# Kernel optimization log

Hardware: AMD Instinct MI355X
Metric: run time of the kernel (lower is better)

The kernel has to match this reference:

```python
import jax, jax.numpy as jnp
import numpy as np

B, C, N = 16, 64, 2048
K, KS, OC = 20, 20, 64
BN_EPS = 1e-5


def setup_inputs() -> dict:
    key = jax.random.key(0)
    k1, k2, k3, k4 = jax.random.split(key, 4)
    feature = jax.random.normal(k1, (B, C, N), dtype=jnp.float32)
    neigh_indexs = jax.random.randint(k2, (B * N, K), 0, B * N, dtype=jnp.int64)
    permatrix = jax.random.normal(k3, (B * N, K, KS), dtype=jnp.float32)
    conv_w = jax.random.normal(k4, (OC, 2 * C), dtype=jnp.float32) * 0.05  # 1x1 conv weight
    conv_b = jnp.zeros((OC,), dtype=jnp.float32)
    gamma = jnp.ones((OC,), dtype=jnp.float32)
    beta = jnp.zeros((OC,), dtype=jnp.float32)
    return {"feature": feature, "neigh_indexs": neigh_indexs, "permatrix": permatrix,
            "conv_w": conv_w, "conv_b": conv_b, "gamma": gamma, "beta": beta}


def _forward(feature, neigh_indexs, permatrix, conv_w, conv_b, gamma, beta):
    bsize, num_feat, num_pts = feature.shape
    # [B, C, N] -> [B*N, C]
    flat = jnp.transpose(feature, (0, 2, 1)).reshape(bsize * num_pts, num_feat)
    # neighbor gather: [B*N, K, C] -> [B*N, C, K]
    feats = jnp.transpose(flat[neigh_indexs], (0, 2, 1))
    f_repeat = jnp.broadcast_to(feats[:, :, 0:1], feats.shape)
    f_relative = feats - f_repeat
    feats = jnp.concatenate([f_repeat, f_relative], axis=1)  # [B*N, 2C, K]
    # per-point small matmul with permutation matrix: [B*N, 2C, KS]
    feats = jnp.einsum('nck,nks->ncs', feats, permatrix)
    # 1x1 conv over channel dim: [B*N, OC, KS]
    out = jnp.einsum('ncs,oc->nos', feats, conv_w) + conv_b[None, :, None]
    # max over neighbors, reshape to [B, OC, N]
    out = jnp.max(out, axis=-1).reshape(bsize, num_pts, -1)
    out = jnp.transpose(out, (0, 2, 1))  # [B, OC, N]
    # BatchNorm1d (training-mode forward: biased var over batch & points)
    mean = jnp.mean(out, axis=(0, 2), keepdims=True)
    var = jnp.var(out, axis=(0, 2), keepdims=True)
    out = (out - mean) * jax.lax.rsqrt(var + BN_EPS)
    return out * gamma[None, :, None] + beta[None, :, None]


def reference(feature, neigh_indexs, permatrix, conv_w, conv_b, gamma, beta):
    return _forward(feature, neigh_indexs, permatrix, conv_w, conv_b, gamma, beta)
```

## Files before the change

### kernel.cpp

```cpp
#include <hip/hip_runtime.h>
#include <hip/hip_fp16.h>

#define B_   16
#define C_   64
#define N_   2048
#define M_   (B_ * N_)
#define K_   20
#define KS_  20
#define OC_  64
#define NWAVE2 8192
#define NBLK2  2048

__global__ __launch_bounds__(256) void k_project(
    const float* __restrict__ feat,
    const float* __restrict__ conv_w,
    __half* __restrict__ ph,
    float*  __restrict__ qf)
{
    const int lane = threadIdx.x & 63;
    const int wg   = blockIdx.x * 4 + (threadIdx.x >> 6);
    float w2[64], wd[64];
    const float4* cw4 = (const float4*)conv_w;
    #pragma unroll
    for (int j = 0; j < 16; ++j) {
        float4 a = cw4[lane * 32 + j];
        float4 b = cw4[lane * 32 + 16 + j];
        w2[4*j+0] = b.x; w2[4*j+1] = b.y; w2[4*j+2] = b.z; w2[4*j+3] = b.w;
        wd[4*j+0] = a.x - b.x; wd[4*j+1] = a.y - b.y;
        wd[4*j+2] = a.z - b.z; wd[4*j+3] = a.w - b.w;
    }
    const int m0 = wg * 16;
    int b0 = m0 >> 11, p0 = m0 & 2047;
    float fv = feat[((size_t)(b0 * 64 + lane)) * 2048 + p0];
    for (int mi = 0; mi < 16; ++mi) {
        const int m = m0 + mi;
        float fnext = 0.f;
        if (mi < 15) {
            const int mn = m + 1;
            fnext = feat[((size_t)((mn >> 11) * 64 + lane)) * 2048 + (mn & 2047)];
        }
        float p0a = 0.f, p1a = 0.f, q0a = 0.f, q1a = 0.f;
        #pragma unroll
        for (int c = 0; c < 32; ++c) {
            float f0 = __int_as_float(
                __builtin_amdgcn_readlane(__float_as_int(fv), c));
            float f1 = __int_as_float(
                __builtin_amdgcn_readlane(__float_as_int(fv), c + 32));
            p0a = fmaf(w2[c], f0, p0a);
            p1a = fmaf(w2[c + 32], f1, p1a);
            q0a = fmaf(wd[c], f0, q0a);
            q1a = fmaf(wd[c + 32], f1, q1a);
        }
        ph[(size_t)m * 64 + lane] = __float2half(p0a + p1a);
        qf[(size_t)m * 64 + lane] = q0a + q1a;
        fv = fnext;
    }
}

typedef float f16v __attribute__((ext_vector_type(16)));

__device__ __forceinline__ float h2f(int u) {
    __half_raw r; r.x = (unsigned short)u;
    return __half2float(__half(r));
}

template<int V, int I>
__device__ __forceinline__ float selv(const f16v& a, const f16v& b,
                                      const f16v& c, const f16v& d,
                                      const f16v& e) {
    if constexpr (V == 0) return a[I];
    else if constexpr (V == 1) return b[I];
    else if constexpr (V == 2) return c[I];
    else if constexpr (V == 3) return d[I];
    else return e[I];
}

template<int KK, bool INIT>
__device__ __forceinline__ void rowfma(float t, float bias, float* acc,
    const f16v& a, const f16v& b, const f16v& c,
    const f16v& d, const f16v& e)
{
    #define RS_(S) { constexpr int e_ = KK * 20 + (S); \
        const float w_ = selv<e_ / 16, e_ % 16>(a, b, c, d, e); \
        acc[S] = fmaf(t, w_, INIT ? bias : acc[S]); }
    RS_(0)  RS_(1)  RS_(2)  RS_(3)  RS_(4)
    RS_(5)  RS_(6)  RS_(7)  RS_(8)  RS_(9)
    RS_(10) RS_(11) RS_(12) RS_(13) RS_(14)
    RS_(15) RS_(16) RS_(17) RS_(18) RS_(19)
    #undef RS_
}

#define CHUNK(tkk, CC, INIT0) { \
    f16v sA, sB, sC, sD, sE; \
    asm volatile("s_load_dwordx16 %0, %1, %2" : "=s"(sA) : "s"(psrc), "n"((CC)*320 +   0)); \
    asm volatile("s_load_dwordx16 %0, %1, %2" : "=s"(sB) : "s"(psrc), "n"((CC)*320 +  64)); \
    asm volatile("s_load_dwordx16 %0, %1, %2" : "=s"(sC) : "s"(psrc), "n"((CC)*320 + 128)); \
    asm volatile("s_load_dwordx16 %0, %1, %2" : "=s"(sD) : "s"(psrc), "n"((CC)*320 + 192)); \
    asm volatile("s_load_dwordx16 %0, %1, %2" : "=s"(sE) : "s"(psrc), "n"((CC)*320 + 256)); \
    asm volatile("s_waitcnt lgkmcnt(0)" \
        : "+s"(sA), "+s"(sB), "+s"(sC), "+s"(sD), "+s"(sE)); \
    rowfma<0, INIT0>(tkk[(CC)*4+0], bias, acc, sA, sB, sC, sD, sE); \
    rowfma<1, false>(tkk[(CC)*4+1], bias, acc, sA, sB, sC, sD, sE); \
    rowfma<2, false>(tkk[(CC)*4+2], bias, acc, sA, sB, sC, sD, sE); \
    rowfma<3, false>(tkk[(CC)*4+3], bias, acc, sA, sB, sC, sD, sE); }

__device__ __forceinline__ void issue_gathers(
    const __half* __restrict__ pht, const float* __restrict__ qft,
    int ivreg, int voff2, int voff4, int (&g)[21])
{
    {
        const int ik0 = __builtin_amdgcn_readlane(ivreg, 0);
        const float* spq = qft + (size_t)(unsigned)ik0 * 64u;
        asm volatile("global_load_dword %0, %1, %2"
                     : "=v"(g[20]) : "v"(voff4), "s"(spq));
    }
    #pragma unroll
    for (int k = 0; k < 20; ++k) {
        const int iku = __builtin_amdgcn_readlane(ivreg, k);
        const __half* sp = pht + (size_t)(unsigned)iku * 64u;
        asm volatile("global_load_ushort %0, %1, %2"
                     : "=v"(g[k]) : "v"(voff2), "s"(sp));
    }
}

#define WAITG(g, CNTTXT) do { \
    asm volatile("s_waitcnt vmcnt(" CNTTXT ")" : \
        "+v"(g[0]),"+v"(g[1]),"+v"(g[2]),"+v"(g[3]),"+v"(g[4]), \
        "+v"(g[5]),"+v"(g[6]),"+v"(g[7]),"+v"(g[8]),"+v"(g[9]), \
        "+v"(g[10]),"+v"(g[11]),"+v"(g[12]),"+v"(g[13]),"+v"(g[14]), \
        "+v"(g[15]),"+v"(g[16]),"+v"(g[17]),"+v"(g[18]),"+v"(g[19]), \
        "+v"(g[20])); \
    __builtin_amdgcn_sched_barrier(0); \
} while (0)

#define COMPUTE(gar, NU) { \
    const float* psrc = perm + (size_t)(NU) * 400; \
    const float qv = __int_as_float(gar[20]); \
    float tk[20]; \
    tk[0]  = h2f(gar[0])  + qv; tk[1]  = h2f(gar[1])  + qv; \
    tk[2]  = h2f(gar[2])  + qv; tk[3]  = h2f(gar[3])  + qv; \
    tk[4]  = h2f(gar[4])  + qv; tk[5]  = h2f(gar[5])  + qv; \
    tk[6]  = h2f(gar[6])  + qv; tk[7]  = h2f(gar[7])  + qv; \
    tk[8]  = h2f(gar[8])  + qv; tk[9]  = h2f(gar[9])  + qv; \
    tk[10] = h2f(gar[10]) + qv; tk[11] = h2f(gar[11]) + qv; \
    tk[12] = h2f(gar[12]) + qv; tk[13] = h2f(gar[13]) + qv; \
    tk[14] = h2f(gar[14]) + qv; tk[15] = h2f(gar[15]) + qv; \
    tk[16] = h2f(gar[16]) + qv; tk[17] = h2f(gar[17]) + qv; \
    tk[18] = h2f(gar[18]) + qv; tk[19] = h2f(gar[19]) + qv; \
    float acc[20]; \
    CHUNK(tk, 0, true) \
    CHUNK(tk, 1, false) \
    CHUNK(tk, 2, false) \
    CHUNK(tk, 3, false) \
    CHUNK(tk, 4, false) \
    float mv = acc[0]; \
    mv = fmaxf(mv, acc[1]);  mv = fmaxf(mv, acc[2]);  mv = fmaxf(mv, acc[3]); \
    mv = fmaxf(mv, acc[4]);  mv = fmaxf(mv, acc[5]);  mv = fmaxf(mv, acc[6]); \
    mv = fmaxf(mv, acc[7]);  mv = fmaxf(mv, acc[8]);  mv = fmaxf(mv, acc[9]); \
    mv = fmaxf(mv, acc[10]); mv = fmaxf(mv, acc[11]); mv = fmaxf(mv, acc[12]); \
    mv = fmaxf(mv, acc[13]); mv = fmaxf(mv, acc[14]); mv = fmaxf(mv, acc[15]); \
    mv = fmaxf(mv, acc[16]); mv = fmaxf(mv, acc[17]); mv = fmaxf(mv, acc[18]); \
    mv = fmaxf(mv, acc[19]); \
    const float* pdst = pre + (size_t)(NU) * 64; \
    asm volatile("global_store_dword %0, %1, %2" \
                 :: "v"(voff4), "v"(mv), "s"(pdst)); \
    sum += mv; \
    sumsq = fmaf(mv, mv, sumsq); }

__global__ __launch_bounds__(256) void k_points(
    const __half* __restrict__ ph,
    const float*  __restrict__ qf,
    const int*    __restrict__ nidx,
    const float*  __restrict__ perm,
    const float*  __restrict__ conv_b,
    float* __restrict__ pre,
    float* __restrict__ partials)
{
    const int tid  = threadIdx.x;
    const int lane = tid & 63;
    const int w    = tid >> 6;
    const int wg   = (int)blockIdx.x * 4 + w;
    const int wgu  = __builtin_amdgcn_readfirstlane(wg);
    const int voff4 = lane * 4;
    const int voff2 = lane * 2;

    float bias = conv_b[lane];
    float sum = 0.f, sumsq = 0.f;

    int iv0 = 0, iv1 = 0, iv2 = 0, iv3 = 0;
    if (lane < 20) {
        iv0 = nidx[(size_t)wgu * K_ + lane];
        iv1 = nidx[((size_t)wgu +     NWAVE2) * K_ + lane];
        iv2 = nidx[((size_t)wgu + 2 * NWAVE2) * K_ + lane];
        iv3 = nidx[((size_t)wgu + 3 * NWAVE2) * K_ + lane];
    }
    asm volatile("s_waitcnt vmcnt(0)"
        : "+v"(bias), "+v"(iv0), "+v"(iv1), "+v"(iv2), "+v"(iv3));
    __builtin_amdgcn_sched_barrier(0);

    int gA[21], gB[21];
    issue_gathers(ph, qf, iv0, voff2, voff4, gA);
    issue_gathers(ph, qf, iv1, voff2, voff4, gB);
    WAITG(gA, "21");
    COMPUTE(gA, wgu)
    issue_gathers(ph, qf, iv2, voff2, voff4, gA);
    WAITG(gB, "22");
    COMPUTE(gB, wgu + NWAVE2)
    issue_gathers(ph, qf, iv3, voff2, voff4, gB);
    WAITG(gA, "22");
    COMPUTE(gA, wgu + 2 * NWAVE2)
    WAITG(gB, "1");
    COMPUTE(gB, wgu + 3 * NWAVE2)

    __shared__ float red[512];
    red[w * 128 + lane]      = sum;
    red[w * 128 + 64 + lane] = sumsq;
    __syncthreads();
    if (tid < 128) {
        float s = red[tid] + red[128 + tid] + red[256 + tid] + red[384 + tid];
        partials[(size_t)blockIdx.x * 128 + tid] = s;
    }
}

#undef COMPUTE
#undef WAITG
#undef CHUNK

__global__ __launch_bounds__(256) void k_stats(
    const float* __restrict__ partials,
    const float* __restrict__ gamma,
    const float* __restrict__ beta,
    float* __restrict__ stats)
{
    const int ch  = blockIdx.x;
    const int tid = threadIdx.x;
    double s = 0.0, s2 = 0.0;
    for (int w = tid; w < NBLK2; w += 256) {
        s  += (double)partials[(size_t)w * 128 + ch];
        s2 += (double)partials[(size_t)w * 128 + 64 + ch];
    }
    __shared__ double sh_s[256];
    __shared__ double sh_q[256];
    sh_s[tid] = s; sh_q[tid] = s2;
    __syncthreads();
    for (int off = 128; off > 0; off >>= 1) {
        if (tid < off) { sh_s[tid] += sh_s[tid + off]; sh_q[tid] += sh_q[tid + off]; }
        __syncthreads();
    }
    if (tid == 0) {
        const double inv_n = 1.0 / (double)M_;
        double mean = sh_s[0] * inv_n;
        double var  = sh_q[0] * inv_n - mean * mean;
        double inv  = 1.0 / sqrt(var + 1e-5);
        double sc   = (double)gamma[ch] * inv;
        stats[ch]      = (float)sc;
        stats[64 + ch] = (float)((double)beta[ch] - mean * sc);
    }
}

__global__ __launch_bounds__(256) void k_apply(
    const float* __restrict__ pre,
    const float* __restrict__ stats,
    float* __restrict__ out)
{
    __shared__ float tile[64 * 65];
    __shared__ float scl[64];
    __shared__ float shf[64];
    const int tid = threadIdx.x;
    if (tid < 64)       scl[tid]      = stats[tid];
    else if (tid < 128) shf[tid - 64] = stats[tid];
    __syncthreads();
    const int b  = blockIdx.x >> 5;
    const int pt = (blockIdx.x & 31) * 64;
    const int c  = tid & 63;
    const int r0 = tid >> 6;
    #pragma unroll
    for (int i = 0; i < 16; ++i) {
        const int r = i * 4 + r0;
        float v = pre[((size_t)(b * 2048 + pt + r)) * 64 + c];
        tile[c * 65 + r] = fmaf(v, scl[c], shf[c]);
    }
    __syncthreads();
    #pragma unroll
    for (int i = 0; i < 16; ++i) {
        const int o = i * 4 + r0;
        out[((size_t)(b * 64 + o)) * 2048 + pt + c] = tile[o * 65 + c];
    }
}

extern "C" void kernel_launch(void* const* d_in, const int* in_sizes, int n_in,
                              void* d_out, int out_size, void* d_ws, size_t ws_size,
                              hipStream_t stream) {
    const float* feat   = (const float*)d_in[0];
    const int*   nidx   = (const int*)  d_in[1];
    const float* perm   = (const float*)d_in[2];
    const float* conv_w = (const float*)d_in[3];
    const float* conv_b = (const float*)d_in[4];
    const float* gamma  = (const float*)d_in[5];
    const float* beta   = (const float*)d_in[6];
    float* out = (float*)d_out;

    char* ws = (char*)d_ws;
    __half* ph      = (__half*)ws;
    float*  qf      = (float*)(ws + (size_t)M_ * 64 * 2);
    float*  pre     = (float*)(ws + (size_t)M_ * 64 * 2
                                  + (size_t)M_ * 64 * 4);
    float*  partials= (float*)(ws + (size_t)M_ * 64 * 2
                                  + (size_t)M_ * 64 * 4 * 2);
    float*  stats   = (float*)(ws + (size_t)M_ * 64 * 2
                                  + (size_t)M_ * 64 * 4 * 2
                                  + (size_t)NBLK2 * 128 * 4);

    hipLaunchKernelGGL(k_project, dim3(512),  dim3(256), 0, stream, feat, conv_w,
                       ph, qf);
    hipLaunchKernelGGL(k_points,  dim3(2048), dim3(256), 0, stream, ph, qf, nidx,
                       perm, conv_b, pre, partials);
    hipLaunchKernelGGL(k_stats,   dim3(64),   dim3(256), 0, stream, partials, gamma,
                       beta, stats);
    hipLaunchKernelGGL(k_apply,   dim3(512),  dim3(256), 0, stream, pre, stats, out);
}
```

Before: 177.0 us.

## Fuse four kernels into one persistent kernel with global atomic barriers

Replaces the four launches (projection, per-point gather/compute, BN stats, apply/transpose) with a single persistent kernel of 1024 blocks. The phases are separated by software grid barriers built on atomic counters, which are cleared by a memset before launch. Each wave now handles 8 points in the gather phase instead of 4, and the projection phase loads its weights in two halves to reduce register pressure. This removes launch gaps and tail effects, but it requires all 1024 blocks to be co-resident (launch_bounds 256,4) or the barriers deadlock, and it adds barrier spin cost.

Measured after the change: 502.5 us. 2.84x slower.

```diff
diff --git a/kernel.cpp b/kernel.cpp
--- a/kernel.cpp
+++ b/kernel.cpp
@@ -8,53 +8,23 @@
 #define K_   20
 #define KS_  20
 #define OC_  64
-#define NWAVE2 8192
-#define NBLK2  2048
-
-__global__ __launch_bounds__(256) void k_project(
-    const float* __restrict__ feat,
-    const float* __restrict__ conv_w,
-    __half* __restrict__ ph,
-    float*  __restrict__ qf)
-{
-    const int lane = threadIdx.x & 63;
-    const int wg   = blockIdx.x * 4 + (threadIdx.x >> 6);
-    float w2[64], wd[64];
-    const float4* cw4 = (const float4*)conv_w;
-    #pragma unroll
-    for (int j = 0; j < 16; ++j) {
-        float4 a = cw4[lane * 32 + j];
-        float4 b = cw4[lane * 32 + 16 + j];
-        w2[4*j+0] = b.x; w2[4*j+1] = b.y; w2[4*j+2] = b.z; w2[4*j+3] = b.w;
-        wd[4*j+0] = a.x - b.x; wd[4*j+1] = a.y - b.y;
-        wd[4*j+2] = a.z - b.z; wd[4*j+3] = a.w - b.w;
-    }
-    const int m0 = wg * 16;
-    int b0 = m0 >> 11, p0 = m0 & 2047;
-    float fv = feat[((size_t)(b0 * 64 + lane)) * 2048 + p0];
-    for (int mi = 0; mi < 16; ++mi) {
-        const int m = m0 + mi;
-        float fnext = 0.f;
-        if (mi < 15) {
-            const int mn = m + 1;
-            fnext = feat[((size_t)((mn >> 11) * 64 + lane)) * 2048 + (mn & 2047)];
-        }
-        float p0a = 0.f, p1a = 0.f, q0a = 0.f, q1a = 0.f;
-        #pragma unroll
-        for (int c = 0; c < 32; ++c) {
-            float f0 = __int_as_float(
-                __builtin_amdgcn_readlane(__float_as_int(fv), c));
-            float f1 = __int_as_float(
-                __builtin_amdgcn_readlane(__float_as_int(fv), c + 32));
-            p0a = fmaf(w2[c], f0, p0a);
-            p1a = fmaf(w2[c + 32], f1, p1a);
-            q0a = fmaf(wd[c], f0, q0a);
-            q1a = fmaf(wd[c + 32], f1, q1a);
-        }
-        ph[(size_t)m * 64 + lane] = __float2half(p0a + p1a);
-        qf[(size_t)m * 64 + lane] = q0a + q1a;
-        fv = fnext;
-    }
+#define NBLKF  1024
+#define NWAVEF 4096
+
+
+__device__ __forceinline__ void gbar(int* cnt, int target) {
+    asm volatile("s_waitcnt vmcnt(0) lgkmcnt(0)" ::: "memory");
+    __syncthreads();
+    if (threadIdx.x == 0) {
+        __threadfence();
+        __hip_atomic_fetch_add(cnt, 1, __ATOMIC_RELAXED,
+                               __HIP_MEMORY_SCOPE_AGENT);
+        while (__hip_atomic_load(cnt, __ATOMIC_RELAXED,
+                                 __HIP_MEMORY_SCOPE_AGENT) < target)
+            __builtin_amdgcn_s_sleep(4);
+        __threadfence();
+    }
+    __syncthreads();
 }
 
 typedef float f16v __attribute__((ext_vector_type(16)));
@@ -90,7 +60,7 @@
     #undef RS_
 }
 
-#define CHUNK(tkk, CC, INIT0) { \
+#define CHUNK(gar, qv, CC, INIT0) { \
     f16v sA, sB, sC, sD, sE; \
     asm volatile("s_load_dwordx16 %0, %1, %2" : "=s"(sA) : "s"(psrc), "n"((CC)*320 +   0)); \
     asm volatile("s_load_dwordx16 %0, %1, %2" : "=s"(sB) : "s"(psrc), "n"((CC)*320 +  64)); \
@@ -99,10 +69,14 @@
     asm volatile("s_load_dwordx16 %0, %1, %2" : "=s"(sE) : "s"(psrc), "n"((CC)*320 + 256)); \
     asm volatile("s_waitcnt lgkmcnt(0)" \
         : "+s"(sA), "+s"(sB), "+s"(sC), "+s"(sD), "+s"(sE)); \
-    rowfma<0, INIT0>(tkk[(CC)*4+0], bias, acc, sA, sB, sC, sD, sE); \
-    rowfma<1, false>(tkk[(CC)*4+1], bias, acc, sA, sB, sC, sD, sE); \
-    rowfma<2, false>(tkk[(CC)*4+2], bias, acc, sA, sB, sC, sD, sE); \
-    rowfma<3, false>(tkk[(CC)*4+3], bias, acc, sA, sB, sC, sD, sE); }
+    const float t0_ = h2f(gar[(CC)*4+0]) + qv; \
+    const float t1_ = h2f(gar[(CC)*4+1]) + qv; \
+    const float t2_ = h2f(gar[(CC)*4+2]) + qv; \
+    const float t3_ = h2f(gar[(CC)*4+3]) + qv; \
+    rowfma<0, INIT0>(t0_, bias, acc, sA, sB, sC, sD, sE); \
+    rowfma<1, false>(t1_, bias, acc, sA, sB, sC, sD, sE); \
+    rowfma<2, false>(t2_, bias, acc, sA, sB, sC, sD, sE); \
+    rowfma<3, false>(t3_, bias, acc, sA, sB, sC, sD, sE); }
 
 __device__ __forceinline__ void issue_gathers(
     const __half* __restrict__ pht, const float* __restrict__ qft,
@@ -136,23 +110,12 @@
 #define COMPUTE(gar, NU) { \
     const float* psrc = perm + (size_t)(NU) * 400; \
     const float qv = __int_as_float(gar[20]); \
-    float tk[20]; \
-    tk[0]  = h2f(gar[0])  + qv; tk[1]  = h2f(gar[1])  + qv; \
-    tk[2]  = h2f(gar[2])  + qv; tk[3]  = h2f(gar[3])  + qv; \
-    tk[4]  = h2f(gar[4])  + qv; tk[5]  = h2f(gar[5])  + qv; \
-    tk[6]  = h2f(gar[6])  + qv; tk[7]  = h2f(gar[7])  + qv; \
-    tk[8]  = h2f(gar[8])  + qv; tk[9]  = h2f(gar[9])  + qv; \
-    tk[10] = h2f(gar[10]) + qv; tk[11] = h2f(gar[11]) + qv; \
-    tk[12] = h2f(gar[12]) + qv; tk[13] = h2f(gar[13]) + qv; \
-    tk[14] = h2f(gar[14]) + qv; tk[15] = h2f(gar[15]) + qv; \
-    tk[16] = h2f(gar[16]) + qv; tk[17] = h2f(gar[17]) + qv; \
-    tk[18] = h2f(gar[18]) + qv; tk[19] = h2f(gar[19]) + qv; \
     float acc[20]; \
-    CHUNK(tk, 0, true) \
-    CHUNK(tk, 1, false) \
-    CHUNK(tk, 2, false) \
-    CHUNK(tk, 3, false) \
-    CHUNK(tk, 4, false) \
+    CHUNK(gar, qv, 0, true) \
+    CHUNK(gar, qv, 1, false) \
+    CHUNK(gar, qv, 2, false) \
+    CHUNK(gar, qv, 3, false) \
+    CHUNK(gar, qv, 4, false) \
     float mv = acc[0]; \
     mv = fmaxf(mv, acc[1]);  mv = fmaxf(mv, acc[2]);  mv = fmaxf(mv, acc[3]); \
     mv = fmaxf(mv, acc[4]);  mv = fmaxf(mv, acc[5]);  mv = fmaxf(mv, acc[6]); \
@@ -167,126 +130,184 @@
     sum += mv; \
     sumsq = fmaf(mv, mv, sumsq); }
 
-__global__ __launch_bounds__(256) void k_points(
-    const __half* __restrict__ ph,
-    const float*  __restrict__ qf,
-    const int*    __restrict__ nidx,
-    const float*  __restrict__ perm,
-    const float*  __restrict__ conv_b,
-    float* __restrict__ pre,
-    float* __restrict__ partials)
+__global__ __launch_bounds__(256, 4) void k_fused(
+    const float* __restrict__ feat,
+    const float* __restrict__ conv_w,
+    const int*   __restrict__ nidx,
+    const float* __restrict__ perm,
+    const float* __restrict__ conv_b,
+    const float* __restrict__ gamma,
+    const float* __restrict__ beta,
+    float* __restrict__ out,
+    __half* __restrict__ ph,
+    float*  __restrict__ qf,
+    float*  __restrict__ pre,
+    float*  __restrict__ partials,
+    float*  __restrict__ stats,
+    int*    __restrict__ barcnt)
 {
     const int tid  = threadIdx.x;
     const int lane = tid & 63;
     const int w    = tid >> 6;
-    const int wg   = (int)blockIdx.x * 4 + w;
-    const int wgu  = __builtin_amdgcn_readfirstlane(wg);
-    const int voff4 = lane * 4;
-    const int voff2 = lane * 2;
-
-    float bias = conv_b[lane];
-    float sum = 0.f, sumsq = 0.f;
-
-    int iv0 = 0, iv1 = 0, iv2 = 0, iv3 = 0;
-    if (lane < 20) {
-        iv0 = nidx[(size_t)wgu * K_ + lane];
-        iv1 = nidx[((size_t)wgu +     NWAVE2) * K_ + lane];
-        iv2 = nidx[((size_t)wgu + 2 * NWAVE2) * K_ + lane];
-        iv3 = nidx[((size_t)wgu + 3 * NWAVE2) * K_ + lane];
-    }
-    asm volatile("s_waitcnt vmcnt(0)"
-        : "+v"(bias), "+v"(iv0), "+v"(iv1), "+v"(iv2), "+v"(iv3));
-    __builtin_amdgcn_sched_barrier(0);
-
-    int gA[21], gB[21];
-    issue_gathers(ph, qf, iv0, voff2, voff4, gA);
-    issue_gathers(ph, qf, iv1, voff2, voff4, gB);
-    WAITG(gA, "21");
-    COMPUTE(gA, wgu)
-    issue_gathers(ph, qf, iv2, voff2, voff4, gA);
-    WAITG(gB, "22");
-    COMPUTE(gB, wgu + NWAVE2)
-    issue_gathers(ph, qf, iv3, voff2, voff4, gB);
-    WAITG(gA, "22");
-    COMPUTE(gA, wgu + 2 * NWAVE2)
-    WAITG(gB, "1");
-    COMPUTE(gB, wgu + 3 * NWAVE2)
-
-    __shared__ float red[512];
-    red[w * 128 + lane]      = sum;
-    red[w * 128 + 64 + lane] = sumsq;
-    __syncthreads();
-    if (tid < 128) {
-        float s = red[tid] + red[128 + tid] + red[256 + tid] + red[384 + tid];
-        partials[(size_t)blockIdx.x * 128 + tid] = s;
+
+    {
+        const int wv = (int)blockIdx.x * 4 + w;
+        const int m0 = wv * 8;
+        const int b0 = m0 >> 11;
+        const float* fb = feat + (size_t)(b0 * 64 + lane) * 2048;
+        const int p0 = m0 & 2047;
+        const float4* cw4 = (const float4*)conv_w;
+        float paq[8], qaq[8];
+        #pragma unroll
+        for (int h = 0; h < 2; ++h) {
+            float w2h[32], wdh[32];
+            #pragma unroll
+            for (int j = 0; j < 8; ++j) {
+                float4 a = cw4[lane * 32 + 8 * h + j];
+                float4 b = cw4[lane * 32 + 16 + 8 * h + j];
+                w2h[4*j+0] = b.x; w2h[4*j+1] = b.y;
+                w2h[4*j+2] = b.z; w2h[4*j+3] = b.w;
+                wdh[4*j+0] = a.x - b.x; wdh[4*j+1] = a.y - b.y;
+                wdh[4*j+2] = a.z - b.z; wdh[4*j+3] = a.w - b.w;
+            }
+            float fv = fb[p0];
+            #pragma unroll
+            for (int mi = 0; mi < 8; ++mi) {
+                float fnext = 0.f;
+                if (mi < 7) fnext = fb[p0 + mi + 1];
+                float pa = 0.f, qa = 0.f;
+                #pragma unroll
+                for (int cc = 0; cc < 32; ++cc) {
+                    float f = __int_as_float(__builtin_amdgcn_readlane(
+                        __float_as_int(fv), 32 * h + cc));
+                    pa = fmaf(w2h[cc], f, pa);
+                    qa = fmaf(wdh[cc], f, qa);
+                }
+                if (h == 0) { paq[mi] = pa; qaq[mi] = qa; }
+                else {
+                    const int m = m0 + mi;
+                    ph[(size_t)m * 64 + lane] = __float2half(paq[mi] + pa);
+                    qf[(size_t)m * 64 + lane] = qaq[mi] + qa;
+                }
+                fv = fnext;
+            }
+        }
+    }
+
+    gbar(barcnt + 0, NBLKF);
+
+    {
+        const int wvu = __builtin_amdgcn_readfirstlane((int)blockIdx.x * 4 + w);
+        const int voff4 = lane * 4;
+        const int voff2 = lane * 2;
+        float bias = conv_b[lane];
+        float sum = 0.f, sumsq = 0.f;
+
+        int iv0=0, iv1=0, iv2=0, iv3=0, iv4=0, iv5=0, iv6=0, iv7=0;
+        if (lane < 20) {
+            iv0 = nidx[((size_t)wvu             ) * K_ + lane];
+            iv1 = nidx[((size_t)wvu +     NWAVEF) * K_ + lane];
+            iv2 = nidx[((size_t)wvu + 2 * NWAVEF) * K_ + lane];
+            iv3 = nidx[((size_t)wvu + 3 * NWAVEF) * K_ + lane];
+            iv4 = nidx[((size_t)wvu + 4 * NWAVEF) * K_ + lane];
+            iv5 = nidx[((size_t)wvu + 5 * NWAVEF) * K_ + lane];
+            iv6 = nidx[((size_t)wvu + 6 * NWAVEF) * K_ + lane];
+            iv7 = nidx[((size_t)wvu + 7 * NWAVEF) * K_ + lane];
+        }
+        asm volatile("s_waitcnt vmcnt(0)"
+            : "+v"(bias), "+v"(iv0), "+v"(iv1), "+v"(iv2), "+v"(iv3),
+              "+v"(iv4), "+v"(iv5), "+v"(iv6), "+v"(iv7));
+        __builtin_amdgcn_sched_barrier(0);
+
+        int gA[21], gB[21];
+        issue_gathers(ph, qf, iv0, voff2, voff4, gA);
+        issue_gathers(ph, qf, iv1, voff2, voff4, gB);
+        WAITG(gA, "21"); COMPUTE(gA, wvu)
+        issue_gathers(ph, qf, iv2, voff2, voff4, gA);
+        WAITG(gB, "22"); COMPUTE(gB, wvu + NWAVEF)
+        issue_gathers(ph, qf, iv3, voff2, voff4, gB);
+        WAITG(gA, "22"); COMPUTE(gA, wvu + 2 * NWAVEF)
+        issue_gathers(ph, qf, iv4, voff2, voff4, gA);
+        WAITG(gB, "22"); COMPUTE(gB, wvu + 3 * NWAVEF)
+        issue_gathers(ph, qf, iv5, voff2, voff4, gB);
+        WAITG(gA, "22"); COMPUTE(gA, wvu + 4 * NWAVEF)
+        issue_gathers(ph, qf, iv6, voff2, voff4, gA);
+        WAITG(gB, "22"); COMPUTE(gB, wvu + 5 * NWAVEF)
+        issue_gathers(ph, qf, iv7, voff2, voff4, gB);
+        WAITG(gA, "22"); COMPUTE(gA, wvu + 6 * NWAVEF)
+        WAITG(gB, "1");  COMPUTE(gB, wvu + 7 * NWAVEF)
+
+        asm volatile("s_waitcnt vmcnt(0)" ::: "memory");
+
+        __shared__ float red[512];
+        red[w * 128 + lane]      = sum;
+        red[w * 128 + 64 + lane] = sumsq;
+        __syncthreads();
+        if (tid < 128) {
+            float s = red[tid] + red[128 + tid] + red[256 + tid] + red[384 + tid];
+            partials[(size_t)blockIdx.x * 128 + tid] = s;
+        }
+    }
+
+    gbar(barcnt + 1, NBLKF);
+
+    if (blockIdx.x < 64) {
+        const int ch = blockIdx.x;
+        double s = 0.0, s2 = 0.0;
+        for (int r = tid; r < NBLKF; r += 256) {
+            s  += (double)partials[(size_t)r * 128 + ch];
+            s2 += (double)partials[(size_t)r * 128 + 64 + ch];
+        }
+        __shared__ double sh_s[256];
+        __shared__ double sh_q[256];
+        sh_s[tid] = s; sh_q[tid] = s2;
+        __syncthreads();
+        for (int off = 128; off > 0; off >>= 1) {
+            if (tid < off) { sh_s[tid] += sh_s[tid + off]; sh_q[tid] += sh_q[tid + off]; }
+            __syncthreads();
+        }
+        if (tid == 0) {
+            const double inv_n = 1.0 / (double)M_;
+            double mean = sh_s[0] * inv_n;
+            double var  = sh_q[0] * inv_n - mean * mean;
+            double inv  = 1.0 / sqrt(var + 1e-5);
+            double sc   = (double)gamma[ch] * inv;
+            stats[ch]      = (float)sc;
+            stats[64 + ch] = (float)((double)beta[ch] - mean * sc);
+        }
+    }
+
+    gbar(barcnt + 2, NBLKF);
+
+    {
+        __shared__ float tile[64 * 33];
+        __shared__ float scl[64];
+        __shared__ float shf[64];
+        if (tid < 64)       scl[tid]      = stats[tid];
+        else if (tid < 128) shf[tid - 64] = stats[tid];
+        __syncthreads();
+        const int b  = blockIdx.x >> 6;
+        const int pt = (blockIdx.x & 63) * 32;
+        const int c  = tid & 63;
+        const int r0 = tid >> 6;
+        #pragma unroll
+        for (int i = 0; i < 8; ++i) {
+            const int r = i * 4 + r0;
+            float v = pre[((size_t)(b * 2048 + pt + r)) * 64 + c];
+            tile[c * 33 + r] = fmaf(v, scl[c], shf[c]);
+        }
+        __syncthreads();
+        const int o  = tid >> 2;
+        const int j0 = (tid & 3) * 8;
+        #pragma unroll
+        for (int j = 0; j < 8; ++j)
+            out[((size_t)(b * 64 + o)) * 2048 + pt + j0 + j] = tile[o * 33 + j0 + j];
     }
 }
 
 #undef COMPUTE
 #undef WAITG
 #undef CHUNK
-
-__global__ __launch_bounds__(256) void k_stats(
-    const float* __restrict__ partials,
-    const float* __restrict__ gamma,
-    const float* __restrict__ beta,
-    float* __restrict__ stats)
-{
-    const int ch  = blockIdx.x;
-    const int tid = threadIdx.x;
-    double s = 0.0, s2 = 0.0;
-    for (int w = tid; w < NBLK2; w += 256) {
-        s  += (double)partials[(size_t)w * 128 + ch];
-        s2 += (double)partials[(size_t)w * 128 + 64 + ch];
-    }
-    __shared__ double sh_s[256];
-    __shared__ double sh_q[256];
-    sh_s[tid] = s; sh_q[tid] = s2;
-    __syncthreads();
-    for (int off = 128; off > 0; off >>= 1) {
-        if (tid < off) { sh_s[tid] += sh_s[tid + off]; sh_q[tid] += sh_q[tid + off]; }
-        __syncthreads();
-    }
-    if (tid == 0) {
-        const double inv_n = 1.0 / (double)M_;
-        double mean = sh_s[0] * inv_n;
-        double var  = sh_q[0] * inv_n - mean * mean;
-        double inv  = 1.0 / sqrt(var + 1e-5);
-        double sc   = (double)gamma[ch] * inv;
-        stats[ch]      = (float)sc;
-        stats[64 + ch] = (float)((double)beta[ch] - mean * sc);
-    }
-}
-
-__global__ __launch_bounds__(256) void k_apply(
-    const float* __restrict__ pre,
-    const float* __restrict__ stats,
-    float* __restrict__ out)
-{
-    __shared__ float tile[64 * 65];
-    __shared__ float scl[64];
-    __shared__ float shf[64];
-    const int tid = threadIdx.x;
-    if (tid < 64)       scl[tid]      = stats[tid];
-    else if (tid < 128) shf[tid - 64] = stats[tid];
-    __syncthreads();
-    const int b  = blockIdx.x >> 5;
-    const int pt = (blockIdx.x & 31) * 64;
-    const int c  = tid & 63;
-    const int r0 = tid >> 6;
-    #pragma unroll
-    for (int i = 0; i < 16; ++i) {
-        const int r = i * 4 + r0;
-        float v = pre[((size_t)(b * 2048 + pt + r)) * 64 + c];
-        tile[c * 65 + r] = fmaf(v, scl[c], shf[c]);
-    }
-    __syncthreads();
-    #pragma unroll
-    for (int i = 0; i < 16; ++i) {
-        const int o = i * 4 + r0;
-        out[((size_t)(b * 64 + o)) * 2048 + pt + c] = tile[o * 65 + c];
-    }
-}
 
 extern "C" void kernel_launch(void* const* d_in, const int* in_sizes, int n_in,
                               void* d_out, int out_size, void* d_ws, size_t ws_size,
@@ -301,21 +322,22 @@
     float* out = (float*)d_out;
 
     char* ws = (char*)d_ws;
-    __half* ph      = (__half*)ws;
-    float*  qf      = (float*)(ws + (size_t)M_ * 64 * 2);
-    float*  pre     = (float*)(ws + (size_t)M_ * 64 * 2
-                                  + (size_t)M_ * 64 * 4);
-    float*  partials= (float*)(ws + (size_t)M_ * 64 * 2
-                                  + (size_t)M_ * 64 * 4 * 2);
-    float*  stats   = (float*)(ws + (size_t)M_ * 64 * 2
-                                  + (size_t)M_ * 64 * 4 * 2
-                                  + (size_t)NBLK2 * 128 * 4);
-
-    hipLaunchKernelGGL(k_project, dim3(512),  dim3(256), 0, stream, feat, conv_w,
-                       ph, qf);
-    hipLaunchKernelGGL(k_points,  dim3(2048), dim3(256), 0, stream, ph, qf, nidx,
-                       perm, conv_b, pre, partials);
-    hipLaunchKernelGGL(k_stats,   dim3(64),   dim3(256), 0, stream, partials, gamma,
-                       beta, stats);
-    hipLaunchKernelGGL(k_apply,   dim3(512),  dim3(256), 0, stream, pre, stats, out);
-}
+    const size_t off_ph   = 0;
+    const size_t off_qf   = off_ph   + (size_t)M_ * 64 * 2;
+    const size_t off_pre  = off_qf   + (size_t)M_ * 64 * 4;
+    const size_t off_par  = off_pre  + (size_t)M_ * 64 * 4;
+    const size_t off_st   = off_par  + (size_t)NBLKF * 128 * 4;
+    const size_t off_cnt  = off_st   + 1024;
+
+    __half* ph       = (__half*)(ws + off_ph);
+    float*  qf       = (float*) (ws + off_qf);
+    float*  pre      = (float*) (ws + off_pre);
+    float*  partials = (float*) (ws + off_par);
+    float*  stats    = (float*) (ws + off_st);
+    int*    barcnt   = (int*)   (ws + off_cnt);
+
+    hipMemsetAsync(barcnt, 0, 3 * sizeof(int), stream);
+    hipLaunchKernelGGL(k_fused, dim3(NBLKF), dim3(256), 0, stream,
+                       feat, conv_w, nidx, perm, conv_b, gamma, beta, out,
+                       ph, qf, pre, partials, stats, barcnt);
+}
```
